# Kernel tuning notes

Measured on AMD Instinct MI355X. Metric: run time of the kernel, lower is better.

## Reference

```python
import jax, jax.numpy as jnp
import numpy as np

NQ = 8            # data qubits: ceil(log2(256))
NLAYERS = 6       # StronglyEntanglingLayers depth
BATCH = 4096
IN_DIM = 2560
ENC_DIM = 256

def leaky(x):
    return jnp.where(x >= 0, x, 0.2 * x)

def rot_mat(phi, theta, omega):
    # PennyLane Rot(phi,theta,omega) = RZ(omega) @ RY(theta) @ RZ(phi)
    c = jnp.cos(theta / 2); s = jnp.sin(theta / 2)
    m00 = jnp.exp(-0.5j * (phi + omega)) * c
    m01 = -jnp.exp(0.5j * (phi - omega)) * s
    m10 = jnp.exp(-0.5j * (phi - omega)) * s
    m11 = jnp.exp(0.5j * (phi + omega)) * c
    return jnp.stack([jnp.stack([m00, m01]), jnp.stack([m10, m11])])

def apply_1q(psi, U, w):
    psi = jnp.tensordot(U, psi, axes=((1,), (w,)))
    return jnp.moveaxis(psi, 0, w)

def apply_cnot(psi, c, t):
    s = jnp.moveaxis(psi, (c, t), (0, 1))
    s = jnp.stack([s[0], s[1, ::-1]], axis=0)
    return jnp.moveaxis(s, (0, 1), (c, t))

def circuit(amps, params):
    # amps: (256,) complex64 normalized amplitudes; params: (L, NQ, 3)
    psi = amps.reshape((2,) * NQ)
    L = params.shape[0]
    for l in range(L):
        for q in range(NQ):
            psi = apply_1q(psi, rot_mat(params[l, q, 0], params[l, q, 1], params[l, q, 2]), q)
        r = l % (NQ - 1) + 1  # PennyLane default imprimitive ranges
        for q in range(NQ):
            psi = apply_cnot(psi, q, (q + r) % NQ)
    probs = jnp.real(psi * jnp.conj(psi))
    z, xm, ym = [], [], []
    yfac_base = jnp.array([-1j, 1j], dtype=psi.dtype)
    for q in range(NQ):
        axes = tuple(i for i in range(NQ) if i != q)
        p = jnp.sum(probs, axis=axes)
        z.append(p[0] - p[1])
        flipped = jnp.flip(psi, axis=q)
        xm.append(jnp.real(jnp.sum(jnp.conj(psi) * flipped)))
        yfac = yfac_base.reshape([2 if i == q else 1 for i in range(NQ)])
        ym.append(jnp.real(jnp.sum(jnp.conj(psi) * (flipped * yfac))))
    return jnp.stack(z + xm + ym)  # (24,) order: Z..., X..., Y...

def forward(x, ew1, eb1, ew2, eb2, ew3, eb3, dec_params,
            dw1, db1, dw2, db2, dw3, db3, dw4, db4, dw5, db5):
    h = leaky(x @ ew1 + eb1)
    h = leaky(h @ ew2 + eb2)
    enc = jnp.tanh(h @ ew3 + eb3)                      # (B, 256)
    nrm = jnp.linalg.norm(enc, axis=1, keepdims=True)
    amps = jax.lax.stop_gradient(enc / jnp.maximum(nrm, 1e-12)).astype(jnp.complex64)
    meas = jax.vmap(lambda a: circuit(a, dec_params))(amps)  # (B, 24)
    h = leaky(meas @ dw1 + db1)
    h = leaky(h @ dw2 + db2)
    h = leaky(h @ dw3 + db3)
    h = leaky(h @ dw4 + db4)
    return jnp.tanh(h @ dw5 + db5)                     # (B, 2560)

def _lin(key, fin, fout):
    k1, k2 = jax.random.split(key)
    lim = 1.0 / np.sqrt(fin)
    w = jax.random.uniform(k1, (fin, fout), jnp.float32, -lim, lim)
    b = jax.random.uniform(k2, (fout,), jnp.float32, -lim, lim)
    return w, b

def setup_inputs() -> dict:
    key = jax.random.key(0)
    ks = jax.random.split(key, 10)
    x = jax.random.normal(ks[0], (BATCH, IN_DIM), jnp.float32)
    ew1, eb1 = _lin(ks[1], IN_DIM, 1024)
    ew2, eb2 = _lin(ks[2], 1024, 512)
    ew3, eb3 = _lin(ks[3], 512, ENC_DIM)
    dec_params = jax.random.uniform(ks[4], (NLAYERS, NQ, 3), jnp.float32, 0.0, 2 * np.pi)
    dw1, db1 = _lin(ks[5], 3 * NQ, 128)
    dw2, db2 = _lin(ks[6], 128, 256)
    dw3, db3 = _lin(ks[7], 256, 512)
    dw4, db4 = _lin(ks[8], 512, 1024)
    dw5, db5 = _lin(ks[9], 1024, IN_DIM)
    return {"x": x, "ew1": ew1, "eb1": eb1, "ew2": ew2, "eb2": eb2, "ew3": ew3, "eb3": eb3,
            "dec_params": dec_params, "dw1": dw1, "db1": db1, "dw2": dw2, "db2": db2,
            "dw3": dw3, "db3": db3, "dw4": dw4, "db4": db4, "dw5": dw5, "db5": db5}

def reference(x, ew1, eb1, ew2, eb2, ew3, eb3, dec_params,
              dw1, db1, dw2, db2, dw3, db3, dw4, db4, dw5, db5):
    return forward(x, ew1, eb1, ew2, eb2, ew3, eb3, dec_params,
                   dw1, db1, dw2, db2, dw3, db3, dw4, db4, dw5, db5)
```

## Files before the change

kernel.cpp:

```cpp
#include <hip/hip_runtime.h>
#include <hip/hip_bf16.h>


using bf16 = __hip_bfloat16;
typedef __attribute__((ext_vector_type(8))) short short8;
typedef __attribute__((ext_vector_type(4))) short short4v;
typedef __attribute__((ext_vector_type(4))) float f32x4;

__device__ inline void stf(float* p, size_t i, float v) { p[i] = v; }
__device__ inline void stf(bf16* p, size_t i, float v) { p[i] = __float2bfloat16(v); }

__device__ inline float fast_tanh(float x) {
  x = fminf(fmaxf(x, -15.0f), 15.0f);
  float t = __expf(2.0f * x);
  return __fdividef(t - 1.0f, t + 1.0f);
}

__device__ inline short f2bs(float x) {
  bf16 h = __float2bfloat16(x);
  return *reinterpret_cast<short*>(&h);
}
__device__ inline short8 ld8b(const float* p) {
  const float4 a = ((const float4*)p)[0];
  const float4 b = ((const float4*)p)[1];
  short8 r;
  r[0] = f2bs(a.x); r[1] = f2bs(a.y); r[2] = f2bs(a.z); r[3] = f2bs(a.w);
  r[4] = f2bs(b.x); r[5] = f2bs(b.y); r[6] = f2bs(b.z); r[7] = f2bs(b.w);
  return r;
}
__device__ inline short4v ld4b(const float* p) {
  const float4 a = *(const float4*)p;
  short4v r;
  r[0] = f2bs(a.x); r[1] = f2bs(a.y); r[2] = f2bs(a.z); r[3] = f2bs(a.w);
  return r;
}

__device__ inline void async_load16(const bf16* g, short* l) {
  __builtin_amdgcn_global_load_lds(
      (const __attribute__((address_space(1))) unsigned int*)g,
      (__attribute__((address_space(3))) unsigned int*)l, 16, 0, 0);
}

__global__ __launch_bounds__(256) void prep_all(
    const float* w0, const float* w1, const float* w2, const float* w3,
    const float* w4, const float* w5, const float* w6, const float* w7,
    const float* b0, const float* b1, const float* b2, const float* b3,
    const float* b4, const float* b5, const float* b6, const float* b7,
    const float* dp, const float* xf,
    bf16* __restrict__ wt, float* __restrict__ biasf, float* __restrict__ gw,
    bf16* __restrict__ xb, int do_x) {
  const int bid = blockIdx.x;
  const int tid = threadIdx.x;
  const int Ks[8]  = {2560, 1024, 512, 24, 128, 256, 512, 1024};
  const int Ns[8]  = {1024, 512, 256, 128, 256, 512, 1024, 2560};
  const int cum[8] = {2560, 3072, 3200, 3204, 3236, 3364, 3876, 6436};
  const long wto[8] = {0, 2621440, 3145728, 3276800, 3280896, 3313664, 3444736, 3969024};
  const float* Wp[8] = {w0, w1, w2, w3, w4, w5, w6, w7};
  const float* Bp[8] = {b0, b1, b2, b3, b4, b5, b6, b7};
  const int boff[8] = {0, 1024, 1536, 1792, 1920, 2176, 2688, 3712};

  if (bid < 6436) {
    int t = 0;
    while (bid >= cum[t]) t++;
    int base = t ? cum[t - 1] : 0;
    int local = bid - base;
    int K = Ks[t], N = Ns[t];
    int tk = (K + 31) >> 5;
    int kt = local % tk, nt = local / tk;
    int Kp = tk << 5;
    __shared__ short tile[32][33];
    int r = tid >> 3, c4 = (tid & 7) << 2;
    int gk = kt * 32 + r, gn = nt * 32 + c4;
    short4v v;
    if (gk < K) v = ld4b(Wp[t] + (size_t)gk * N + gn);
    else { v[0] = 0; v[1] = 0; v[2] = 0; v[3] = 0; }
    tile[r][c4] = v[0]; tile[r][c4 + 1] = v[1]; tile[r][c4 + 2] = v[2]; tile[r][c4 + 3] = v[3];
    __syncthreads();
    int n = tid >> 3, k4 = (tid & 7) << 2;
    short4v o;
    o[0] = tile[k4][n]; o[1] = tile[k4 + 1][n]; o[2] = tile[k4 + 2][n]; o[3] = tile[k4 + 3][n];
    *(short4v*)&wt[wto[t] + (size_t)(nt * 32 + n) * Kp + kt * 32 + k4] = o;
  } else if (bid < 6444) {
    int b = bid - 6436;
    int nb = Ns[b];
    for (int t2 = tid; t2 < nb; t2 += 256)
      biasf[boff[b] + t2] = Bp[b][t2];
  } else if (bid == 6444) {
    int g = tid;
    if (g < 48) {
      float phi = dp[g * 3 + 0], theta = dp[g * 3 + 1], omega = dp[g * 3 + 2];
      float c = cosf(0.5f * theta), s = sinf(0.5f * theta);
      float a = 0.5f * (phi + omega), d = 0.5f * (phi - omega);
      float ca = cosf(a), sa = sinf(a), cd = cosf(d), sd = sinf(d);
      float* o = gw + g * 8;
      o[0] =  ca * c; o[1] = -sa * c;
      o[2] = -cd * s; o[3] = -sd * s;
      o[4] =  cd * s; o[5] = -sd * s;
      o[6] =  ca * c; o[7] =  sa * c;
    }
  } else if (do_x) {
    long i = ((long)(bid - 6445) * 256 + tid) * 8;
    if (i < 10485760L) {
      short8 v = ld8b(xf + i);
      *(short8*)((short*)xb + i) = v;
    }
  }
}

template <int BM, int BN, int BK, int WR, int WC, int ACT, typename TC>
__global__ __launch_bounds__(256) void gemm_async(const bf16* __restrict__ A,
                                                  const bf16* __restrict__ Bt,
                                                  const float* __restrict__ bias,
                                                  TC* __restrict__ C,
                                                  int M, int N, int K) {
  constexpr int CPR = BK / 8;
  constexpr int MASK = CPR - 1;
  constexpr int RPW = 64 / CPR;
  constexpr int RPP = 4 * RPW;
  constexpr int WMT = BM / WR;
  constexpr int WNT = BN / WC;
  constexpr int FI = WMT / 16;
  constexpr int FJ = WNT / 16;
  constexpr int KK = BK / 32;
  __shared__ __align__(16) short As[2][BM * BK];
  __shared__ __align__(16) short Bs[2][BN * BK];
  const int tid = threadIdx.x;
  const int lane = tid & 63;
  const int wid = tid >> 6;
  const int wm = wid / WC, wn = wid % WC;
  const int bm = blockIdx.y * BM;
  const int bn = blockIdx.x * BN;

  const int st_r = lane / CPR;
  const int st_cs = (lane & MASK) ^ (st_r & MASK);

  const int frag_m = lane & 15;
  const int q = lane >> 4;

  auto stage = [&](int buf, int k0) {
#pragma unroll
    for (int p = 0; p < BM / RPP; ++p) {
      const bf16* g = A + (size_t)(bm + p * RPP + wid * RPW + st_r) * K + k0 + st_cs * 8;
      async_load16(g, &As[buf][(p * RPP + wid * RPW) * BK]);
    }
#pragma unroll
    for (int p = 0; p < BN / RPP; ++p) {
      const bf16* g = Bt + (size_t)(bn + p * RPP + wid * RPW + st_r) * K + k0 + st_cs * 8;
      async_load16(g, &Bs[buf][(p * RPP + wid * RPW) * BK]);
    }
  };

  f32x4 acc[FI][FJ] = {};

  stage(0, 0);
  __syncthreads();

  const int nsteps = K / BK;
  int cur = 0;
  for (int t = 0; t < nsteps; ++t) {
    if (t + 1 < nsteps) stage(cur ^ 1, (t + 1) * BK);

    short8 af[FI][KK], bfr[FJ][KK];
#pragma unroll
    for (int i = 0; i < FI; ++i) {
      const int m = wm * WMT + i * 16 + frag_m;
#pragma unroll
      for (int kk = 0; kk < KK; ++kk) {
        const int slot = (kk * 4 + q) ^ (m & MASK);
        af[i][kk] = *(const short8*)&As[cur][m * BK + slot * 8];
      }
    }
#pragma unroll
    for (int j = 0; j < FJ; ++j) {
      const int n = wn * WNT + j * 16 + frag_m;
#pragma unroll
      for (int kk = 0; kk < KK; ++kk) {
        const int slot = (kk * 4 + q) ^ (n & MASK);
        bfr[j][kk] = *(const short8*)&Bs[cur][n * BK + slot * 8];
      }
    }
#pragma unroll
    for (int kk = 0; kk < KK; ++kk)
#pragma unroll
      for (int i = 0; i < FI; ++i)
#pragma unroll
        for (int j = 0; j < FJ; ++j)
          acc[i][j] = __builtin_amdgcn_mfma_f32_16x16x32_bf16(af[i][kk], bfr[j][kk], acc[i][j], 0, 0, 0);

    __syncthreads();
    cur ^= 1;
  }

  const int col_lane = lane & 15;
  const int row_quad = q << 2;
#pragma unroll
  for (int i = 0; i < FI; ++i) {
#pragma unroll
    for (int j = 0; j < FJ; ++j) {
      int n = bn + wn * WNT + j * 16 + col_lane;
      float bj = bias[n];
#pragma unroll
      for (int r = 0; r < 4; ++r) {
        int m = bm + wm * WMT + i * 16 + row_quad + r;
        float v = acc[i][j][r] + bj;
        if (ACT == 0) v = (v >= 0.f) ? v : 0.2f * v;
        else v = fast_tanh(v);
        stf(C, (size_t)m * N + n, v);
      }
    }
  }
}

__global__ __launch_bounds__(256) void gemm_cvt(const float* __restrict__ A,
                                                const float* __restrict__ W,
                                                const float* __restrict__ bias,
                                                bf16* __restrict__ C,
                                                int M, int N, int K) {
  __shared__ __align__(16) short As[128 * 40];
  __shared__ __align__(16) short Bs[128 * 40];
  const int tid = threadIdx.x;
  const int lane = tid & 63;
  const int wave = tid >> 6;
  const int wm = wave >> 1, wn = wave & 1;
  const int bm = blockIdx.y * 128;
  const int bn = blockIdx.x * 128;
  const int a_row0 = tid >> 2;
  const int a_kcol = (tid & 3) << 3;
  const int b_ncol = (tid & 31) << 2;
  const int b_krow = (tid >> 5) << 2;
  const int frag_m = lane & 15;
  const int frag_k = (lane >> 4) << 3;

  f32x4 acc[4][4] = {};

  for (int k0 = 0; k0 < K; k0 += 32) {
#pragma unroll
    for (int c = 0; c < 2; ++c) {
      const int row = c * 64 + a_row0;
      short8 v = ld8b(A + (size_t)(bm + row) * K + k0 + a_kcol);
      *(short8*)&As[row * 40 + a_kcol] = v;
    }
    short4v bv[4];
#pragma unroll
    for (int kk = 0; kk < 4; ++kk)
      bv[kk] = ld4b(W + (size_t)(k0 + b_krow + kk) * N + bn + b_ncol);
#pragma unroll
    for (int nn = 0; nn < 4; ++nn) {
      short4v w;
      w[0] = bv[0][nn]; w[1] = bv[1][nn]; w[2] = bv[2][nn]; w[3] = bv[3][nn];
      *(short4v*)&Bs[(b_ncol + nn) * 40 + b_krow] = w;
    }
    __syncthreads();
    short8 af[4], bfr[4];
#pragma unroll
    for (int i = 0; i < 4; ++i)
      af[i] = *(const short8*)&As[(wm * 64 + i * 16 + frag_m) * 40 + frag_k];
#pragma unroll
    for (int j = 0; j < 4; ++j)
      bfr[j] = *(const short8*)&Bs[(wn * 64 + j * 16 + frag_m) * 40 + frag_k];
#pragma unroll
    for (int i = 0; i < 4; ++i)
#pragma unroll
      for (int j = 0; j < 4; ++j)
        acc[i][j] = __builtin_amdgcn_mfma_f32_16x16x32_bf16(af[i], bfr[j], acc[i][j], 0, 0, 0);
    __syncthreads();
  }

  const int col_lane = lane & 15;
  const int row_quad = (lane >> 4) << 2;
#pragma unroll
  for (int i = 0; i < 4; ++i)
#pragma unroll
    for (int j = 0; j < 4; ++j) {
      int n = bn + wn * 64 + j * 16 + col_lane;
      float bj = bias[n];
#pragma unroll
      for (int r = 0; r < 4; ++r) {
        int m = bm + wm * 64 + i * 16 + row_quad + r;
        float v = acc[i][j][r] + bj;
        v = (v >= 0.f) ? v : 0.2f * v;
        stf(C, (size_t)m * N + n, v);
      }
    }
}

__global__ __launch_bounds__(256) void circuit_wave(const float* __restrict__ enc,
                                                    const float* __restrict__ gw,
                                                    const float* __restrict__ dw1,
                                                    const float* __restrict__ db1,
                                                    bf16* __restrict__ d1out) {
  __shared__ float gsh[384];
  const int tid = threadIdx.x;
  for (int t = tid; t < 384; t += 256) gsh[t] = gw[t];
  __syncthreads();
  const int lane = tid & 63;
  const int b = blockIdx.x * 4 + (tid >> 6);

  float4 e = *(const float4*)(enc + (size_t)b * 256 + lane * 4);
  float re[4] = {e.x, e.y, e.z, e.w};
  float im[4] = {0.f, 0.f, 0.f, 0.f};
  float ss = e.x * e.x + e.y * e.y + e.z * e.z + e.w * e.w;
#pragma unroll
  for (int o = 32; o; o >>= 1) ss += __shfl_xor(ss, o, 64);
  float inv = 1.0f / fmaxf(sqrtf(ss), 1e-12f);
#pragma unroll
  for (int j = 0; j < 4; ++j) re[j] *= inv;

  for (int l = 0; l < 6; ++l) {
    for (int qq = 0; qq < 8; ++qq) {
      const float* g = &gsh[(l * 8 + qq) * 8];
      const int s = 1 << (7 - qq);
      if (s >= 4) {
        const int lm = s >> 2;
        const bool hi = (lane & lm) != 0;
        const float g0r = hi ? g[4] : g[0], g0i = hi ? g[5] : g[1];
        const float g1r = hi ? g[6] : g[2], g1i = hi ? g[7] : g[3];
#pragma unroll
        for (int j = 0; j < 4; ++j) {
          float orr = __shfl_xor(re[j], lm, 64);
          float oii = __shfl_xor(im[j], lm, 64);
          float p0r = hi ? orr : re[j], p0i = hi ? oii : im[j];
          float p1r = hi ? re[j] : orr, p1i = hi ? im[j] : oii;
          re[j] = g0r * p0r - g0i * p0i + g1r * p1r - g1i * p1i;
          im[j] = g0r * p0i + g0i * p0r + g1r * p1i + g1i * p1r;
        }
      } else {
#pragma unroll
        for (int j0 = 0; j0 < 4; ++j0) {
          if ((j0 & s) == 0) {
            int j1 = j0 | s;
            float p0r = re[j0], p0i = im[j0], p1r = re[j1], p1i = im[j1];
            re[j0] = g[0] * p0r - g[1] * p0i + g[2] * p1r - g[3] * p1i;
            im[j0] = g[0] * p0i + g[1] * p0r + g[2] * p1i + g[3] * p1r;
            re[j1] = g[4] * p0r - g[5] * p0i + g[6] * p1r - g[7] * p1i;
            im[j1] = g[4] * p0i + g[5] * p0r + g[6] * p1i + g[7] * p1r;
          }
        }
      }
    }
    const int r = l % 7 + 1;
    for (int qq = 0; qq < 8; ++qq) {
      const int sc = 1 << (7 - qq);
      const int st = 1 << (7 - ((qq + r) & 7));
      if (st >= 4) {
        const int lm = st >> 2;
        if (sc >= 4) {
          const bool ctl = (lane & (sc >> 2)) != 0;
#pragma unroll
          for (int j = 0; j < 4; ++j) {
            float orr = __shfl_xor(re[j], lm, 64);
            float oii = __shfl_xor(im[j], lm, 64);
            re[j] = ctl ? orr : re[j];
            im[j] = ctl ? oii : im[j];
          }
        } else {
#pragma unroll
          for (int j = 0; j < 4; ++j) {
            if (j & sc) {
              re[j] = __shfl_xor(re[j], lm, 64);
              im[j] = __shfl_xor(im[j], lm, 64);
            }
          }
        }
      } else {
        if (sc >= 4) {
          const bool ctl = (lane & (sc >> 2)) != 0;
#pragma unroll
          for (int j0 = 0; j0 < 4; ++j0) {
            if ((j0 & st) == 0) {
              int j1 = j0 | st;
              float t0r = re[j0], t0i = im[j0];
              float t1r = re[j1], t1i = im[j1];
              re[j0] = ctl ? t1r : t0r; im[j0] = ctl ? t1i : t0i;
              re[j1] = ctl ? t0r : t1r; im[j1] = ctl ? t0i : t1i;
            }
          }
        } else {
#pragma unroll
          for (int j0 = 0; j0 < 4; ++j0) {
            if ((j0 & sc) && (j0 & st) == 0) {
              int j1 = j0 | st;
              float tr = re[j0], ti = im[j0];
              re[j0] = re[j1]; im[j0] = im[j1];
              re[j1] = tr; im[j1] = ti;
            }
          }
        }
      }
    }
  }

  float mz[8], mx[8], my[8];
#pragma unroll
  for (int qq = 0; qq < 8; ++qq) {
    const int s = 1 << (7 - qq);
    float z = 0.f, x = 0.f, y = 0.f;
#pragma unroll
    for (int j = 0; j < 4; ++j) {
      float fr, fi;
      if (s >= 4) {
        fr = __shfl_xor(re[j], s >> 2, 64);
        fi = __shfl_xor(im[j], s >> 2, 64);
      } else {
        fr = re[j ^ s]; fi = im[j ^ s];
      }
      float prob = re[j] * re[j] + im[j] * im[j];
      int i = lane * 4 + j;
      float sg = (i & s) ? -1.f : 1.f;
      z += sg * prob;
      x += re[j] * fr + im[j] * fi;
      y += sg * (re[j] * fi - im[j] * fr);
    }
#pragma unroll
    for (int o = 32; o; o >>= 1) {
      z += __shfl_xor(z, o, 64);
      x += __shfl_xor(x, o, 64);
      y += __shfl_xor(y, o, 64);
    }
    mz[qq] = z; mx[qq] = x; my[qq] = y;
  }

#pragma unroll
  for (int half = 0; half < 2; ++half) {
    const int n = lane + half * 64;
    float acc = db1[n];
#pragma unroll
    for (int qq = 0; qq < 8; ++qq) {
      acc += mz[qq] * dw1[qq * 128 + n];
      acc += mx[qq] * dw1[(8 + qq) * 128 + n];
      acc += my[qq] * dw1[(16 + qq) * 128 + n];
    }
    acc = (acc >= 0.f) ? acc : 0.2f * acc;
    d1out[(size_t)b * 128 + n] = __float2bfloat16(acc);
  }
}

extern "C" void kernel_launch(void* const* d_in, const int* in_sizes, int n_in,
                              void* d_out, int out_size, void* d_ws, size_t ws_size,
                              hipStream_t stream) {
  (void)in_sizes; (void)n_in; (void)out_size;
  char* wsb = (char*)d_ws;
  float* gw    = (float*)(wsb + 256);
  float* biasf = (float*)(wsb + 4096);
  float* encf  = (float*)(wsb + 294912);
  bf16*  P     = (bf16*)(wsb + 4489216);
  bf16*  Q     = (bf16*)(wsb + 12877824);
  bf16*  WT    = (bf16*)(wsb + 17072128);
  bf16*  Xb    = (bf16*)(wsb + 30253056);
  const bool have_xb = ws_size >= 51224576;

  bf16* ew1t = WT + 0;
  bf16* ew2t = WT + 2621440;
  bf16* ew3t = WT + 3145728;
  bf16* dw2t = WT + 3280896;
  bf16* dw3t = WT + 3313664;
  bf16* dw4t = WT + 3444736;
  bf16* dw5t = WT + 3969024;
  float* beb1 = biasf + 0;
  float* beb2 = biasf + 1024;
  float* beb3 = biasf + 1536;
  float* bdb2 = biasf + 1920;
  float* bdb3 = biasf + 2176;
  float* bdb4 = biasf + 2688;
  float* bdb5 = biasf + 3712;

  prep_all<<<11565, 256, 0, stream>>>(
      (const float*)d_in[1], (const float*)d_in[3], (const float*)d_in[5],
      (const float*)d_in[8], (const float*)d_in[10], (const float*)d_in[12],
      (const float*)d_in[14], (const float*)d_in[16],
      (const float*)d_in[2], (const float*)d_in[4], (const float*)d_in[6],
      (const float*)d_in[9], (const float*)d_in[11], (const float*)d_in[13],
      (const float*)d_in[15], (const float*)d_in[17],
      (const float*)d_in[7], (const float*)d_in[0],
      WT, biasf, gw, Xb, have_xb ? 1 : 0);

  if (have_xb) {
    gemm_async<128, 64, 64, 4, 1, 0, bf16><<<dim3(16, 32), 256, 0, stream>>>(
        Xb, ew1t, beb1, P, 4096, 1024, 2560);
  } else {
    gemm_cvt<<<dim3(8, 32), 256, 0, stream>>>(
        (const float*)d_in[0], (const float*)d_in[1], beb1, P, 4096, 1024, 2560);
  }

  gemm_async<64, 64, 64, 2, 2, 0, bf16><<<dim3(8, 64), 256, 0, stream>>>(
      P, ew2t, beb2, Q, 4096, 512, 1024);
  gemm_async<64, 64, 64, 2, 2, 1, float><<<dim3(4, 64), 256, 0, stream>>>(
      Q, ew3t, beb3, encf, 4096, 256, 512);

  circuit_wave<<<1024, 256, 0, stream>>>(encf, gw, (const float*)d_in[8],
                                         (const float*)d_in[9], Q);

  gemm_async<64, 64, 64, 2, 2, 0, bf16><<<dim3(4, 64), 256, 0, stream>>>(
      Q, dw2t, bdb2, P, 4096, 256, 128);
  gemm_async<64, 64, 64, 2, 2, 0, bf16><<<dim3(8, 64), 256, 0, stream>>>(
      P, dw3t, bdb3, Q, 4096, 512, 256);
  gemm_async<128, 64, 64, 4, 1, 0, bf16><<<dim3(16, 32), 256, 0, stream>>>(
      Q, dw4t, bdb4, P, 4096, 1024, 512);
  gemm_async<128, 128, 64, 2, 2, 1, float><<<dim3(20, 32), 256, 0, stream>>>(
      P, dw5t, bdb5, (float*)d_out, 4096, 2560, 1024);
}
```

Baseline: 301.0 us.

## Replace per-sample circuit simulation with precomputed unitary applied via split-bf16 GEMM

The fixed quantum circuit is turned into its 256x256 complex unitary, computed once in prep_all by running each basis vector through the circuit and stored as hi/lo bf16 splits. The per-sample state evolution then becomes a GEMM: the encoder's last layer writes tanh outputs as [hi, lo, hi] bf16 blocks, a GEMM of K=768 produces real and imaginary amplitudes, and a new meas_d1 kernel normalises and computes the expectation values plus the first decoder layer. This is meant to replace the shuffle-heavy per-sample gate simulation with MFMA work, at the cost of an extra GEMM pass, an fp32 intermediate state buffer, and accuracy that depends on the split-bf16 emulation.

```diff
diff --git a/kernel.cpp b/kernel.cpp
--- a/kernel.cpp
+++ b/kernel.cpp
@@ -41,6 +41,93 @@
       (__attribute__((address_space(3))) unsigned int*)l, 16, 0, 0);
 }
 
+__device__ inline void run_circuit(float (&re)[4], float (&im)[4],
+                                   const float* gsh, int lane) {
+  for (int l = 0; l < 6; ++l) {
+    for (int qq = 0; qq < 8; ++qq) {
+      const float* g = &gsh[(l * 8 + qq) * 8];
+      const int s = 1 << (7 - qq);
+      if (s >= 4) {
+        const int lm = s >> 2;
+        const bool hi = (lane & lm) != 0;
+        const float g0r = hi ? g[4] : g[0], g0i = hi ? g[5] : g[1];
+        const float g1r = hi ? g[6] : g[2], g1i = hi ? g[7] : g[3];
+#pragma unroll
+        for (int j = 0; j < 4; ++j) {
+          float orr = __shfl_xor(re[j], lm, 64);
+          float oii = __shfl_xor(im[j], lm, 64);
+          float p0r = hi ? orr : re[j], p0i = hi ? oii : im[j];
+          float p1r = hi ? re[j] : orr, p1i = hi ? im[j] : oii;
+          re[j] = g0r * p0r - g0i * p0i + g1r * p1r - g1i * p1i;
+          im[j] = g0r * p0i + g0i * p0r + g1r * p1i + g1i * p1r;
+        }
+      } else {
+#pragma unroll
+        for (int j0 = 0; j0 < 4; ++j0) {
+          if ((j0 & s) == 0) {
+            int j1 = j0 | s;
+            float p0r = re[j0], p0i = im[j0], p1r = re[j1], p1i = im[j1];
+            re[j0] = g[0] * p0r - g[1] * p0i + g[2] * p1r - g[3] * p1i;
+            im[j0] = g[0] * p0i + g[1] * p0r + g[2] * p1i + g[3] * p1r;
+            re[j1] = g[4] * p0r - g[5] * p0i + g[6] * p1r - g[7] * p1i;
+            im[j1] = g[4] * p0i + g[5] * p0r + g[6] * p1i + g[7] * p1r;
+          }
+        }
+      }
+    }
+    const int r = l % 7 + 1;
+    for (int qq = 0; qq < 8; ++qq) {
+      const int sc = 1 << (7 - qq);
+      const int st = 1 << (7 - ((qq + r) & 7));
+      if (st >= 4) {
+        const int lm = st >> 2;
+        if (sc >= 4) {
+          const bool ctl = (lane & (sc >> 2)) != 0;
+#pragma unroll
+          for (int j = 0; j < 4; ++j) {
+            float orr = __shfl_xor(re[j], lm, 64);
+            float oii = __shfl_xor(im[j], lm, 64);
+            re[j] = ctl ? orr : re[j];
+            im[j] = ctl ? oii : im[j];
+          }
+        } else {
+#pragma unroll
+          for (int j = 0; j < 4; ++j) {
+            if (j & sc) {
+              re[j] = __shfl_xor(re[j], lm, 64);
+              im[j] = __shfl_xor(im[j], lm, 64);
+            }
+          }
+        }
+      } else {
+        if (sc >= 4) {
+          const bool ctl = (lane & (sc >> 2)) != 0;
+#pragma unroll
+          for (int j0 = 0; j0 < 4; ++j0) {
+            if ((j0 & st) == 0) {
+              int j1 = j0 | st;
+              float t0r = re[j0], t0i = im[j0];
+              float t1r = re[j1], t1i = im[j1];
+              re[j0] = ctl ? t1r : t0r; im[j0] = ctl ? t1i : t0i;
+              re[j1] = ctl ? t0r : t1r; im[j1] = ctl ? t0i : t1i;
+            }
+          }
+        } else {
+#pragma unroll
+          for (int j0 = 0; j0 < 4; ++j0) {
+            if ((j0 & sc) && (j0 & st) == 0) {
+              int j1 = j0 | st;
+              float tr = re[j0], ti = im[j0];
+              re[j0] = re[j1]; im[j0] = im[j1];
+              re[j1] = tr; im[j1] = ti;
+            }
+          }
+        }
+      }
+    }
+  }
+}
+
 __global__ __launch_bounds__(256) void prep_all(
     const float* w0, const float* w1, const float* w2, const float* w3,
     const float* w4, const float* w5, const float* w6, const float* w7,
@@ -48,9 +135,50 @@
     const float* b4, const float* b5, const float* b6, const float* b7,
     const float* dp, const float* xf,
     bf16* __restrict__ wt, float* __restrict__ biasf, float* __restrict__ gw,
-    bf16* __restrict__ xb, int do_x) {
-  const int bid = blockIdx.x;
+    bf16* __restrict__ xb, bf16* __restrict__ btu, int do_x) {
+  int bid = blockIdx.x;
   const int tid = threadIdx.x;
+
+  if (bid < 64) {
+    __shared__ float gsh[384];
+    if (tid < 48) {
+      float phi = dp[tid * 3 + 0], theta = dp[tid * 3 + 1], omega = dp[tid * 3 + 2];
+      float c = cosf(0.5f * theta), s = sinf(0.5f * theta);
+      float a = 0.5f * (phi + omega), d = 0.5f * (phi - omega);
+      float ca = cosf(a), sa = sinf(a), cd = cosf(d), sd = sinf(d);
+      float* o = &gsh[tid * 8];
+      o[0] =  ca * c; o[1] = -sa * c;
+      o[2] = -cd * s; o[3] = -sd * s;
+      o[4] =  cd * s; o[5] = -sd * s;
+      o[6] =  ca * c; o[7] =  sa * c;
+    }
+    __syncthreads();
+    const int lane = tid & 63;
+    const int col = bid * 4 + (tid >> 6);
+    float re[4], im[4];
+#pragma unroll
+    for (int j = 0; j < 4; ++j) { re[j] = (lane * 4 + j == col) ? 1.f : 0.f; im[j] = 0.f; }
+    run_circuit(re, im, gsh, lane);
+#pragma unroll
+    for (int j = 0; j < 4; ++j) {
+      int n = lane * 4 + j;
+      {
+        bf16 h = __float2bfloat16(re[j]);
+        float lo = re[j] - __bfloat162float(h);
+        size_t base = (size_t)n * 768 + col;
+        btu[base] = h; btu[base + 256] = h; btu[base + 512] = __float2bfloat16(lo);
+      }
+      {
+        bf16 h = __float2bfloat16(im[j]);
+        float lo = im[j] - __bfloat162float(h);
+        size_t base = (size_t)(256 + n) * 768 + col;
+        btu[base] = h; btu[base + 256] = h; btu[base + 512] = __float2bfloat16(lo);
+      }
+    }
+    return;
+  }
+  bid -= 64;
+
   const int Ks[8]  = {2560, 1024, 512, 24, 128, 256, 512, 1024};
   const int Ns[8]  = {1024, 512, 256, 128, 256, 512, 1024, 2560};
   const int cum[8] = {2560, 3072, 3200, 3204, 3236, 3364, 3876, 6436};
@@ -198,14 +326,27 @@
 #pragma unroll
     for (int j = 0; j < FJ; ++j) {
       int n = bn + wn * WNT + j * 16 + col_lane;
-      float bj = bias[n];
+      float bj = (ACT == 2) ? 0.f : bias[n];
 #pragma unroll
       for (int r = 0; r < 4; ++r) {
         int m = bm + wm * WMT + i * 16 + row_quad + r;
         float v = acc[i][j][r] + bj;
-        if (ACT == 0) v = (v >= 0.f) ? v : 0.2f * v;
-        else v = fast_tanh(v);
-        stf(C, (size_t)m * N + n, v);
+        if (ACT == 0) {
+          v = (v >= 0.f) ? v : 0.2f * v;
+          stf(C, (size_t)m * N + n, v);
+        } else if (ACT == 1) {
+          stf(C, (size_t)m * N + n, fast_tanh(v));
+        } else if (ACT == 2) {
+          stf(C, (size_t)m * N + n, v);
+        } else {
+          float tv = fast_tanh(v);
+          bf16 h = __float2bfloat16(tv);
+          float lo = tv - __bfloat162float(h);
+          size_t base = (size_t)m * 768 + n;
+          ((bf16*)C)[base] = h;
+          ((bf16*)C)[base + 256] = __float2bfloat16(lo);
+          ((bf16*)C)[base + 512] = h;
+        }
       }
     }
   }
@@ -284,6 +425,72 @@
     }
 }
 
+__global__ __launch_bounds__(256) void meas_d1(const float* __restrict__ PSI,
+                                               const float* __restrict__ dw1,
+                                               const float* __restrict__ db1,
+                                               bf16* __restrict__ d1out) {
+  const int tid = threadIdx.x;
+  const int lane = tid & 63;
+  const int b = blockIdx.x * 4 + (tid >> 6);
+
+  const float* pp = PSI + (size_t)b * 512;
+  float4 ar = *(const float4*)(pp + lane * 4);
+  float4 ai = *(const float4*)(pp + 256 + lane * 4);
+  float re[4] = {ar.x, ar.y, ar.z, ar.w};
+  float im[4] = {ai.x, ai.y, ai.z, ai.w};
+
+  float ss = 0.f;
+#pragma unroll
+  for (int j = 0; j < 4; ++j) ss += re[j] * re[j] + im[j] * im[j];
+#pragma unroll
+  for (int o = 32; o; o >>= 1) ss += __shfl_xor(ss, o, 64);
+  const float inv = 1.0f / fmaxf(ss, 1e-24f);
+
+  float mz[8], mx[8], my[8];
+#pragma unroll
+  for (int qq = 0; qq < 8; ++qq) {
+    const int s = 1 << (7 - qq);
+    float z = 0.f, x = 0.f, y = 0.f;
+#pragma unroll
+    for (int j = 0; j < 4; ++j) {
+      float fr, fi;
+      if (s >= 4) {
+        fr = __shfl_xor(re[j], s >> 2, 64);
+        fi = __shfl_xor(im[j], s >> 2, 64);
+      } else {
+        fr = re[j ^ s]; fi = im[j ^ s];
+      }
+      float prob = re[j] * re[j] + im[j] * im[j];
+      int i = lane * 4 + j;
+      float sg = (i & s) ? -1.f : 1.f;
+      z += sg * prob;
+      x += re[j] * fr + im[j] * fi;
+      y += sg * (re[j] * fi - im[j] * fr);
+    }
+#pragma unroll
+    for (int o = 32; o; o >>= 1) {
+      z += __shfl_xor(z, o, 64);
+      x += __shfl_xor(x, o, 64);
+      y += __shfl_xor(y, o, 64);
+    }
+    mz[qq] = z * inv; mx[qq] = x * inv; my[qq] = y * inv;
+  }
+
+#pragma unroll
+  for (int half = 0; half < 2; ++half) {
+    const int n = lane + half * 64;
+    float acc = db1[n];
+#pragma unroll
+    for (int qq = 0; qq < 8; ++qq) {
+      acc += mz[qq] * dw1[qq * 128 + n];
+      acc += mx[qq] * dw1[(8 + qq) * 128 + n];
+      acc += my[qq] * dw1[(16 + qq) * 128 + n];
+    }
+    acc = (acc >= 0.f) ? acc : 0.2f * acc;
+    d1out[(size_t)b * 128 + n] = __float2bfloat16(acc);
+  }
+}
+
 __global__ __launch_bounds__(256) void circuit_wave(const float* __restrict__ enc,
                                                     const float* __restrict__ gw,
                                                     const float* __restrict__ dw1,
@@ -306,89 +513,7 @@
 #pragma unroll
   for (int j = 0; j < 4; ++j) re[j] *= inv;
 
-  for (int l = 0; l < 6; ++l) {
-    for (int qq = 0; qq < 8; ++qq) {
-      const float* g = &gsh[(l * 8 + qq) * 8];
-      const int s = 1 << (7 - qq);
-      if (s >= 4) {
-        const int lm = s >> 2;
-        const bool hi = (lane & lm) != 0;
-        const float g0r = hi ? g[4] : g[0], g0i = hi ? g[5] : g[1];
-        const float g1r = hi ? g[6] : g[2], g1i = hi ? g[7] : g[3];
-#pragma unroll
-        for (int j = 0; j < 4; ++j) {
-          float orr = __shfl_xor(re[j], lm, 64);
-          float oii = __shfl_xor(im[j], lm, 64);
-          float p0r = hi ? orr : re[j], p0i = hi ? oii : im[j];
-          float p1r = hi ? re[j] : orr, p1i = hi ? im[j] : oii;
-          re[j] = g0r * p0r - g0i * p0i + g1r * p1r - g1i * p1i;
-          im[j] = g0r * p0i + g0i * p0r + g1r * p1i + g1i * p1r;
-        }
-      } else {
-#pragma unroll
-        for (int j0 = 0; j0 < 4; ++j0) {
-          if ((j0 & s) == 0) {
-            int j1 = j0 | s;
-            float p0r = re[j0], p0i = im[j0], p1r = re[j1], p1i = im[j1];
-            re[j0] = g[0] * p0r - g[1] * p0i + g[2] * p1r - g[3] * p1i;
-            im[j0] = g[0] * p0i + g[1] * p0r + g[2] * p1i + g[3] * p1r;
-            re[j1] = g[4] * p0r - g[5] * p0i + g[6] * p1r - g[7] * p1i;
-            im[j1] = g[4] * p0i + g[5] * p0r + g[6] * p1i + g[7] * p1r;
-          }
-        }
-      }
-    }
-    const int r = l % 7 + 1;
-    for (int qq = 0; qq < 8; ++qq) {
-      const int sc = 1 << (7 - qq);
-      const int st = 1 << (7 - ((qq + r) & 7));
-      if (st >= 4) {
-        const int lm = st >> 2;
-        if (sc >= 4) {
-          const bool ctl = (lane & (sc >> 2)) != 0;
-#pragma unroll
-          for (int j = 0; j < 4; ++j) {
-            float orr = __shfl_xor(re[j], lm, 64);
-            float oii = __shfl_xor(im[j], lm, 64);
-            re[j] = ctl ? orr : re[j];
-            im[j] = ctl ? oii : im[j];
-          }
-        } else {
-#pragma unroll
-          for (int j = 0; j < 4; ++j) {
-            if (j & sc) {
-              re[j] = __shfl_xor(re[j], lm, 64);
-              im[j] = __shfl_xor(im[j], lm, 64);
-            }
-          }
-        }
-      } else {
-        if (sc >= 4) {
-          const bool ctl = (lane & (sc >> 2)) != 0;
-#pragma unroll
-          for (int j0 = 0; j0 < 4; ++j0) {
-            if ((j0 & st) == 0) {
-              int j1 = j0 | st;
-              float t0r = re[j0], t0i = im[j0];
-              float t1r = re[j1], t1i = im[j1];
-              re[j0] = ctl ? t1r : t0r; im[j0] = ctl ? t1i : t0i;
-              re[j1] = ctl ? t0r : t1r; im[j1] = ctl ? t0i : t1i;
-            }
-          }
-        } else {
-#pragma unroll
-          for (int j0 = 0; j0 < 4; ++j0) {
-            if ((j0 & sc) && (j0 & st) == 0) {
-              int j1 = j0 | st;
-              float tr = re[j0], ti = im[j0];
-              re[j0] = re[j1]; im[j0] = im[j1];
-              re[j1] = tr; im[j1] = ti;
-            }
-          }
-        }
-      }
-    }
-  }
+  run_circuit(re, im, gsh, lane);
 
   float mz[8], mx[8], my[8];
 #pragma unroll
@@ -443,10 +568,13 @@
   float* gw    = (float*)(wsb + 256);
   float* biasf = (float*)(wsb + 4096);
   float* encf  = (float*)(wsb + 294912);
+  bf16*  BtU   = (bf16*)(wsb + 294912);
   bf16*  P     = (bf16*)(wsb + 4489216);
   bf16*  Q     = (bf16*)(wsb + 12877824);
   bf16*  WT    = (bf16*)(wsb + 17072128);
   bf16*  Xb    = (bf16*)(wsb + 30253056);
+  bf16*  Ap    = (bf16*)(wsb + 30253056);
+  float* PSI   = (float*)(wsb + 36544512);
   const bool have_xb = ws_size >= 51224576;
 
   bf16* ew1t = WT + 0;
@@ -464,7 +592,7 @@
   float* bdb4 = biasf + 2688;
   float* bdb5 = biasf + 3712;
 
-  prep_all<<<11565, 256, 0, stream>>>(
+  prep_all<<<11629, 256, 0, stream>>>(
       (const float*)d_in[1], (const float*)d_in[3], (const float*)d_in[5],
       (const float*)d_in[8], (const float*)d_in[10], (const float*)d_in[12],
       (const float*)d_in[14], (const float*)d_in[16],
@@ -472,7 +600,7 @@
       (const float*)d_in[9], (const float*)d_in[11], (const float*)d_in[13],
       (const float*)d_in[15], (const float*)d_in[17],
       (const float*)d_in[7], (const float*)d_in[0],
-      WT, biasf, gw, Xb, have_xb ? 1 : 0);
+      WT, biasf, gw, Xb, BtU, have_xb ? 1 : 0);
 
   if (have_xb) {
     gemm_async<128, 64, 64, 4, 1, 0, bf16><<<dim3(16, 32), 256, 0, stream>>>(
@@ -484,11 +612,20 @@
 
   gemm_async<64, 64, 64, 2, 2, 0, bf16><<<dim3(8, 64), 256, 0, stream>>>(
       P, ew2t, beb2, Q, 4096, 512, 1024);
-  gemm_async<64, 64, 64, 2, 2, 1, float><<<dim3(4, 64), 256, 0, stream>>>(
-      Q, ew3t, beb3, encf, 4096, 256, 512);
-
-  circuit_wave<<<1024, 256, 0, stream>>>(encf, gw, (const float*)d_in[8],
-                                         (const float*)d_in[9], Q);
+
+  if (have_xb) {
+    gemm_async<64, 64, 64, 2, 2, 3, bf16><<<dim3(4, 64), 256, 0, stream>>>(
+        Q, ew3t, beb3, Ap, 4096, 256, 512);
+    gemm_async<64, 64, 64, 2, 2, 2, float><<<dim3(8, 64), 256, 0, stream>>>(
+        Ap, BtU, beb3 , PSI, 4096, 512, 768);
+    meas_d1<<<1024, 256, 0, stream>>>(PSI, (const float*)d_in[8],
+                                      (const float*)d_in[9], Q);
+  } else {
+    gemm_async<64, 64, 64, 2, 2, 1, float><<<dim3(4, 64), 256, 0, stream>>>(
+        Q, ew3t, beb3, encf, 4096, 256, 512);
+    circuit_wave<<<1024, 256, 0, stream>>>(encf, gw, (const float*)d_in[8],
+                                           (const float*)d_in[9], Q);
+  }
 
   gemm_async<64, 64, 64, 2, 2, 0, bf16><<<dim3(4, 64), 256, 0, stream>>>(
       Q, dw2t, bdb2, P, 4096, 256, 128);
```

After: 299.0 us. About the same (-0.7%).
